# Performance work log

Hardware: AMD Instinct MI355X
Metric: run time of the kernel (lower is better)

The kernel has to match this reference:

```python
import jax, jax.numpy as jnp
import numpy as np

N = 100000   # nodes
E = 1600000  # edges
H = 8        # heads
D = 16       # per-head dim
HD = H * D   # 128 = hidden_dim * num_heads == input_dim
G = 128      # graphs in batch
OUT = 64     # output_dim
EPS = 1e-3   # BatchNorm eps
NEG_SLOPE = 0.2
THRESH = 0.5


def setup_inputs() -> dict:
    key = jax.random.key(0)
    ks = jax.random.split(key, 20)
    rn = lambda k, s: jax.random.normal(k, s, jnp.float32) * 0.1
    return {
        "h": jax.random.normal(ks[0], (N, HD), jnp.float32),
        "src": jax.random.randint(ks[1], (E,), 0, N),
        "dst": jax.random.randint(ks[2], (E,), 0, N),
        "graph_ids": jnp.sort(jax.random.randint(ks[3], (N,), 0, G)),
        # GAT layer 0 params
        "W0": rn(ks[4], (HD, HD)), "al0": rn(ks[5], (H, D)), "ar0": rn(ks[6], (H, D)), "b0": rn(ks[7], (HD,)),
        "g0": jnp.ones((HD,), jnp.float32), "be0": jnp.zeros((HD,), jnp.float32),
        # GAT layer 1 params
        "W1": rn(ks[8], (HD, HD)), "al1": rn(ks[9], (H, D)), "ar1": rn(ks[10], (H, D)), "b1": rn(ks[11], (HD,)),
        "g1": jnp.ones((HD,), jnp.float32), "be1": jnp.zeros((HD,), jnp.float32),
        # MaskLinear prediction head
        "pred_W": rn(ks[12], (OUT, HD)), "pred_b": rn(ks[13], (OUT,)),
        "mask_real": jax.random.uniform(ks[14], (OUT, HD), jnp.float32),
    }


def _gat(h, W, al, ar, b, src, dst):
    # DGL GATConv: fc -> per-node attn halves -> edge LeakyReLU -> segment softmax over dst -> scatter-add
    feat = (h @ W).reshape(N, H, D)                 # [N,H,D]
    el = jnp.sum(feat * al, axis=-1)                # [N,H]
    er = jnp.sum(feat * ar, axis=-1)                # [N,H]
    e = jax.nn.leaky_relu(el[src] + er[dst], NEG_SLOPE)  # [E,H]
    emax = jax.ops.segment_max(e, dst, num_segments=N)   # [N,H]
    ee = jnp.exp(e - emax[dst])
    denom = jax.ops.segment_sum(ee, dst, num_segments=N) # [N,H]
    a = ee / denom[dst]                             # [E,H]
    msg = a[:, :, None] * feat[src]                 # [E,H,D]
    out = jax.ops.segment_sum(msg, dst, num_segments=N)  # [N,H,D]
    return out.reshape(N, HD) + b


def _bn(x, g, be):
    mu = jnp.mean(x, axis=0)
    var = jnp.mean((x - mu) ** 2, axis=0)
    return (x - mu) * jax.lax.rsqrt(var + EPS) * g + be


def reference(h, src, dst, graph_ids, W0, al0, ar0, b0, g0, be0,
              W1, al1, ar1, b1, g1, be1, pred_W, pred_b, mask_real):
    # layer 0: GAT -> BN -> ReLU (no residual)
    h1 = jax.nn.relu(_bn(_gat(h, W0, al0, ar0, b0, src, dst), g0, be0))
    # layer 1: GAT -> BN -> ReLU + residual
    h2 = jax.nn.relu(_bn(_gat(h1, W1, al1, ar1, b1, src, dst), g1, be1)) + h1
    # SumPooling over graphs in the batch
    pooled = jax.ops.segment_sum(h2, graph_ids, num_segments=G)  # [G,HD]
    # MaskLinear with binarized mask (eval path, no dropout)
    mask = (mask_real > THRESH).astype(pooled.dtype)
    return pooled @ (pred_W * mask).T + pred_b  # [G,OUT]
```

## Files before the change

kernel.cpp:

```cpp
#include <hip/hip_runtime.h>
#include <cstdint>

#define N_NODES 100000
#define N_EDGES 1600000
#define H 8
#define D 16
#define HD 128
#define G_GRAPHS 128
#define OUT_DIM 64
#define EPS 1e-3f
#define NEG 0.2f
#define NBUCK 196
#define BSHIFT 9
#define BCAP 10240
#define MT 64
#define APAD 136
#define NTILES 1563
#define GEMM_GRID 512
#define BNP_ROWS 64
#define BNS_ROWS 128
#define WTROWS 144
#define SRCMASK 0x1FFFF

typedef __attribute__((ext_vector_type(8))) short bf16x8;
typedef __attribute__((ext_vector_type(4))) float f32x4;
typedef __attribute__((ext_vector_type(8))) unsigned short u16x8;

__device__ __forceinline__ unsigned short f2bf(float x) {
    unsigned u = __float_as_uint(x);
    unsigned r = (u + 0x7FFFu + ((u >> 16) & 1u)) >> 16;
    return (unsigned short)r;
}
__device__ __forceinline__ float plo(unsigned q) {
    return __uint_as_float(q << 16);
}
__device__ __forceinline__ float phi(unsigned q) {
    return __uint_as_float(q & 0xFFFF0000u);
}
__device__ __forceinline__ unsigned packbf(float a, float b) {
    return (unsigned)f2bf(a) | ((unsigned)f2bf(b) << 16);
}

__global__ void convert_wt(const float* __restrict__ W0, const float* __restrict__ W1,
                           const float* __restrict__ al0, const float* __restrict__ ar0,
                           const float* __restrict__ al1, const float* __restrict__ ar1,
                           unsigned short* __restrict__ Wt0, unsigned short* __restrict__ Wt1,
                           int* __restrict__ bucketCnt, float* __restrict__ pooled,
                           float* __restrict__ sums01) {
    int t = blockIdx.x * blockDim.x + threadIdx.x;
    if (t < NBUCK) bucketCnt[t] = 0;
    if (t < 512) sums01[t] = 0.f;
    for (int i = t; i < G_GRAPHS * HD; i += gridDim.x * blockDim.x) pooled[i] = 0.f;
    if (t < HD * HD) {
        int k = t >> 7, n = t & 127;
        Wt0[n * HD + k] = f2bf(W0[t]);
        Wt1[n * HD + k] = f2bf(W1[t]);
        return;
    }
    int u = t - HD * HD;
    if (u < HD * 16) {
        int k = u >> 4, j = u & 15;
        int h = j & 7;
        const float* a0 = (j < 8) ? al0 : ar0;
        const float* a1 = (j < 8) ? al1 : ar1;
        float s0 = 0.f, s1 = 0.f;
#pragma unroll
        for (int d = 0; d < 16; ++d) {
            s0 += W0[k * HD + h * 16 + d] * a0[h * 16 + d];
            s1 += W1[k * HD + h * 16 + d] * a1[h * 16 + d];
        }
        Wt0[(HD + j) * HD + k] = f2bf(s0);
        Wt1[(HD + j) * HD + k] = f2bf(s1);
    }
}

__global__ __launch_bounds__(256) void bucket_scatter(const int4* __restrict__ src4,
                                                      const int4* __restrict__ dst4,
                                                      int* __restrict__ bucketCnt,
                                                      int* __restrict__ pairs) {
    __shared__ int hist[NBUCK];
    __shared__ int cur[NBUCK];
    int t = threadIdx.x;
    if (t < NBUCK) hist[t] = 0;
    __syncthreads();
    int base4 = blockIdx.x * 1024;
    const int NE4 = N_EDGES / 4;
    int4 s[4], d[4];
    int valid[4];
#pragma unroll
    for (int k = 0; k < 4; ++k) {
        int i4 = base4 + t + k * 256;
        if (i4 < NE4) {
            s[k] = src4[i4];
            d[k] = dst4[i4];
            valid[k] = 1;
            atomicAdd(&hist[d[k].x >> BSHIFT], 1);
            atomicAdd(&hist[d[k].y >> BSHIFT], 1);
            atomicAdd(&hist[d[k].z >> BSHIFT], 1);
            atomicAdd(&hist[d[k].w >> BSHIFT], 1);
        } else {
            valid[k] = 0;
        }
    }
    __syncthreads();
    if (t < NBUCK) {
        int c = hist[t];
        cur[t] = (c > 0) ? atomicAdd(&bucketCnt[t], c) : 0;
    }
    __syncthreads();
#pragma unroll
    for (int k = 0; k < 4; ++k) {
        if (valid[k]) {
            int ss[4] = {s[k].x, s[k].y, s[k].z, s[k].w};
            int dd[4] = {d[k].x, d[k].y, d[k].z, d[k].w};
#pragma unroll
            for (int j = 0; j < 4; ++j) {
                int b = dd[j] >> BSHIFT;
                int slot = atomicAdd(&cur[b], 1);
                pairs[(size_t)b * BCAP + slot] = ((dd[j] & 511) << 17) | ss[j];
            }
        }
    }
}

__global__ __launch_bounds__(256) void bucket_finish(const int* __restrict__ bucketCnt,
                                                     const int* __restrict__ pairs,
                                                     int2* __restrict__ ninfo,
                                                     int* __restrict__ csr_src) {
    __shared__ int hist[512];
    __shared__ int loc[512];
    __shared__ int bufA[256], bufB[256];
    __shared__ int bbase_sh;
    int b = blockIdx.x, t = threadIdx.x;
    int mycnt = bucketCnt[b];
    int base0 = b << BSHIFT;

    bufA[t] = (t < NBUCK) ? bucketCnt[t] : 0;
    __syncthreads();
    {
        int* a = bufA; int* bb = bufB;
        for (int off = 1; off < 256; off <<= 1) {
            int val = a[t];
            if (t >= off) val += a[t - off];
            bb[t] = val;
            __syncthreads();
            int* c = a; a = bb; bb = c;
        }
        if (t == 0) bbase_sh = a[b] - mycnt;
    }
    hist[t] = 0;
    hist[t + 256] = 0;
    __syncthreads();
    {
        const int4* p4 = (const int4*)&pairs[(size_t)b * BCAP];
        int n4 = mycnt >> 2;
        for (int i = t; i < n4; i += 256) {
            int4 w = p4[i];
            atomicAdd(&hist[(unsigned)w.x >> 17], 1);
            atomicAdd(&hist[(unsigned)w.y >> 17], 1);
            atomicAdd(&hist[(unsigned)w.z >> 17], 1);
            atomicAdd(&hist[(unsigned)w.w >> 17], 1);
        }
        for (int i = (n4 << 2) + t; i < mycnt; i += 256)
            atomicAdd(&hist[(unsigned)pairs[(size_t)b * BCAP + i] >> 17], 1);
    }
    __syncthreads();
    int s0 = hist[2 * t], s1 = hist[2 * t + 1];
    int ps = s0 + s1;
    bufA[t] = ps;
    __syncthreads();
    int total_excl;
    {
        int* a = bufA; int* bb = bufB;
        for (int off = 1; off < 256; off <<= 1) {
            int val = a[t];
            if (t >= off) val += a[t - off];
            bb[t] = val;
            __syncthreads();
            int* c = a; a = bb; bb = c;
        }
        total_excl = a[t] - ps;
    }
    int bbase = bbase_sh;
    loc[2 * t] = total_excl;
    loc[2 * t + 1] = total_excl + s0;
    int n0 = base0 + 2 * t, n1 = base0 + 2 * t + 1;
    if (n0 < N_NODES) ninfo[n0] = make_int2(bbase + total_excl, s0);
    if (n1 < N_NODES) ninfo[n1] = make_int2(bbase + total_excl + s0, s1);
    __syncthreads();
    {
        const int4* p4 = (const int4*)&pairs[(size_t)b * BCAP];
        int n4 = mycnt >> 2;
        for (int i = t; i < n4; i += 256) {
            int4 w = p4[i];
            int ws[4] = {w.x, w.y, w.z, w.w};
#pragma unroll
            for (int j = 0; j < 4; ++j) {
                int dl = (unsigned)ws[j] >> 17;
                int r = atomicAdd(&loc[dl], 1);
                csr_src[bbase + r] = ws[j] & SRCMASK;
            }
        }
        for (int i = (n4 << 2) + t; i < mycnt; i += 256) {
            int w = pairs[(size_t)b * BCAP + i];
            int dl = (unsigned)w >> 17;
            int r = atomicAdd(&loc[dl], 1);
            csr_src[bbase + r] = w & SRCMASK;
        }
    }
}

template <int MODE>
__global__ __launch_bounds__(256, 2) void gemm_mfma(const void* __restrict__ Xv,
                                                    const unsigned short* __restrict__ Wt,
                                                    unsigned short* __restrict__ Yb,
                                                    float* __restrict__ el,
                                                    float* __restrict__ er,
                                                    int nrows,
                                                    const float* __restrict__ sums,
                                                    const float* __restrict__ gam,
                                                    const float* __restrict__ bet) {
    __shared__ unsigned short As[MT * APAD];
    __shared__ __align__(16) float scs[HD];
    __shared__ __align__(16) float shs[HD];
    int tid = threadIdx.x;
    int wave = tid >> 6, lane = tid & 63;
    int qd = lane >> 4, l16 = lane & 15;

    if (MODE == 1) {
        if (tid < HD) {
            float invN = 1.0f / (float)N_NODES;
            float mu = sums[tid] * invN;
            float rs = rsqrtf(sums[HD + tid] * invN - mu * mu + EPS);
            float sc = rs * gam[tid];
            scs[tid] = sc;
            shs[tid] = bet[tid] - mu * sc;
        }
        __syncthreads();
    }

    bf16x8 bfr[9][4];
#pragma unroll
    for (int nt = 0; nt < 9; ++nt)
#pragma unroll
        for (int kb = 0; kb < 4; ++kb)
            bfr[nt][kb] = *(const bf16x8*)&Wt[(nt * 16 + l16) * HD + kb * 32 + qd * 8];

    int srow = tid >> 2, scol = (tid & 3) * 32;

    for (int t = blockIdx.x; t < NTILES; t += gridDim.x) {
        int rbase = t * MT;
        {
            int gr = rbase + srow;
            u16x8 o[4];
            if (gr < nrows) {
                if (MODE == 0) {
                    const float* X = (const float*)Xv;
#pragma unroll
                    for (int i = 0; i < 4; ++i) {
                        float4 va = *(const float4*)&X[(size_t)gr * HD + scol + i * 8];
                        float4 vb = *(const float4*)&X[(size_t)gr * HD + scol + i * 8 + 4];
                        o[i][0] = f2bf(va.x); o[i][1] = f2bf(va.y);
                        o[i][2] = f2bf(va.z); o[i][3] = f2bf(va.w);
                        o[i][4] = f2bf(vb.x); o[i][5] = f2bf(vb.y);
                        o[i][6] = f2bf(vb.z); o[i][7] = f2bf(vb.w);
                    }
                } else {
                    const unsigned* X32 = (const unsigned*)Xv;
#pragma unroll
                    for (int i = 0; i < 4; ++i) {
                        uint4 u = *(const uint4*)&X32[(size_t)gr * 64 + (scol >> 1) + i * 4];
                        f32x4 sa = *(const f32x4*)&scs[scol + i * 8];
                        f32x4 sb = *(const f32x4*)&scs[scol + i * 8 + 4];
                        f32x4 ha = *(const f32x4*)&shs[scol + i * 8];
                        f32x4 hb = *(const f32x4*)&shs[scol + i * 8 + 4];
                        float z0 = fmaxf(plo(u.x) * sa.x + ha.x, 0.f);
                        float z1 = fmaxf(phi(u.x) * sa.y + ha.y, 0.f);
                        float z2 = fmaxf(plo(u.y) * sa.z + ha.z, 0.f);
                        float z3 = fmaxf(phi(u.y) * sa.w + ha.w, 0.f);
                        float z4 = fmaxf(plo(u.z) * sb.x + hb.x, 0.f);
                        float z5 = fmaxf(phi(u.z) * sb.y + hb.y, 0.f);
                        float z6 = fmaxf(plo(u.w) * sb.z + hb.z, 0.f);
                        float z7 = fmaxf(phi(u.w) * sb.w + hb.w, 0.f);
                        o[i][0] = f2bf(z0); o[i][1] = f2bf(z1);
                        o[i][2] = f2bf(z2); o[i][3] = f2bf(z3);
                        o[i][4] = f2bf(z4); o[i][5] = f2bf(z5);
                        o[i][6] = f2bf(z6); o[i][7] = f2bf(z7);
                    }
                }
            } else {
#pragma unroll
                for (int i = 0; i < 4; ++i) o[i] = (u16x8)0;
            }
#pragma unroll
            for (int i = 0; i < 4; ++i)
                *(u16x8*)&As[srow * APAD + scol + i * 8] = o[i];
        }
        __syncthreads();
        f32x4 acc[9];
#pragma unroll
        for (int nt = 0; nt < 9; ++nt) acc[nt] = (f32x4){0.f, 0.f, 0.f, 0.f};
        bf16x8 afr[4];
#pragma unroll
        for (int kb = 0; kb < 4; ++kb)
            afr[kb] = *(const bf16x8*)&As[(wave * 16 + l16) * APAD + kb * 32 + qd * 8];
#pragma unroll
        for (int nt = 0; nt < 9; ++nt)
#pragma unroll
            for (int kb = 0; kb < 4; ++kb)
                acc[nt] = __builtin_amdgcn_mfma_f32_16x16x32_bf16(afr[kb], bfr[nt][kb], acc[nt], 0, 0, 0);
        int orow = rbase + wave * 16 + qd * 4;
        if (orow + 3 < nrows) {
#pragma unroll
            for (int nt = 0; nt < 8; ++nt)
#pragma unroll
                for (int r = 0; r < 4; ++r)
                    Yb[(size_t)(orow + r) * HD + nt * 16 + l16] = f2bf(acc[nt][r]);
#pragma unroll
            for (int r = 0; r < 4; ++r) {
                float v = acc[8][r];
                if (l16 < 8) el[(orow + r) * 8 + l16] = v;
                else er[(orow + r) * 8 + (l16 - 8)] = v;
            }
        } else {
#pragma unroll
            for (int nt = 0; nt < 8; ++nt)
                for (int r = 0; r < 4; ++r)
                    if (orow + r < nrows)
                        Yb[(size_t)(orow + r) * HD + nt * 16 + l16] = f2bf(acc[nt][r]);
            for (int r = 0; r < 4; ++r) {
                if (orow + r < nrows) {
                    float v = acc[8][r];
                    if (l16 < 8) el[(orow + r) * 8 + l16] = v;
                    else er[(orow + r) * 8 + (l16 - 8)] = v;
                }
            }
        }
        __syncthreads();
    }
}

__global__ __launch_bounds__(256) void gat_node(const int2* __restrict__ ninfo,
                                                const int* __restrict__ csr_src,
                                                const float* __restrict__ el,
                                                const float* __restrict__ er,
                                                const uint2* __restrict__ featq,
                                                unsigned* __restrict__ gatb) {
    int node = blockIdx.x * 4 + (threadIdx.x >> 6);
    if (node >= N_NODES) return;
    int lane = threadIdx.x & 63;
    int h7 = lane & 7;
    int eidx = lane >> 3;
    int l32 = lane & 31;
    int hacc = l32 >> 2;
    int half = lane >> 5;
    int ibase = half * 8 + hacc;

    int2 pd = ninfo[node];
    int p = pd.x;
    int cnt = pd.y;
    float ern = er[node * 8 + h7];
    float ds = 0.f, a0 = 0.f, a1 = 0.f, a2 = 0.f, a3 = 0.f;

    int nfull = cnt & ~7;
    if (nfull) {
        int s = csr_src[p + eidx];
        float x = el[(unsigned)s * 8u + h7];
        int c = 0;
        for (;;) {
            float v = x + ern;
            v = fmaxf(v, NEG * v);
            float e = __expf(v);
            ds += e;
            int cn = c + 8;
            int snext = 0; float xnext = 0.f;
            if (cn < nfull) {
                snext = csr_src[p + cn + eidx];
                xnext = el[(unsigned)snext * 8u + h7];
            }
#pragma unroll
            for (int k = 0; k < 4; ++k) {
                float ek = __shfl(e, ibase + 16 * k);
                int sk = __shfl(s, ibase + 16 * k);
                uint2 q = featq[(size_t)((unsigned)sk * 32u + (unsigned)l32)];
                a0 += ek * plo(q.x); a1 += ek * phi(q.x);
                a2 += ek * plo(q.y); a3 += ek * phi(q.y);
            }
            if (cn >= nfull) break;
            c = cn; s = snext; x = xnext;
        }
    }
    int rem = cnt & 7;
    if (rem) {
        int s = 0; float e = 0.f;
        if (eidx < rem) {
            s = csr_src[p + nfull + eidx];
            float v = el[(unsigned)s * 8u + h7] + ern;
            v = fmaxf(v, NEG * v);
            e = __expf(v);
        }
        ds += e;
        int nst = (rem + 1) >> 1;
        for (int k = 0; k < nst; ++k) {
            float ek = __shfl(e, ibase + 16 * k);
            int sk = __shfl(s, ibase + 16 * k);
            uint2 q = featq[(size_t)((unsigned)sk * 32u + (unsigned)l32)];
            a0 += ek * plo(q.x); a1 += ek * phi(q.x);
            a2 += ek * plo(q.y); a3 += ek * phi(q.y);
        }
    }
    ds += __shfl_xor(ds, 8);
    ds += __shfl_xor(ds, 16);
    ds += __shfl_xor(ds, 32);
    float dfull = __shfl(ds, hacc);
    float invd = dfull > 0.f ? 1.f / dfull : 0.f;
    a0 += __shfl_xor(a0, 32);
    a1 += __shfl_xor(a1, 32);
    a2 += __shfl_xor(a2, 32);
    a3 += __shfl_xor(a3, 32);
    if (half == 0) {
        uint2 w;
        w.x = packbf(a0 * invd, a1 * invd);
        w.y = packbf(a2 * invd, a3 * invd);
        ((uint2*)gatb)[(size_t)node * 32 + l32] = w;
    }
}

__global__ __launch_bounds__(256) void bn_stats(const unsigned* __restrict__ xb,
                                                float* __restrict__ sums, int nrows) {
    int cp = threadIdx.x & 63;
    int rr = threadIdx.x >> 6;
    int r0 = blockIdx.x * BNS_ROWS;
    int rend = r0 + BNS_ROWS < nrows ? r0 + BNS_ROWS : nrows;
    float s0 = 0.f, q0 = 0.f, s1 = 0.f, q1 = 0.f;
    for (int r = r0 + rr; r < rend; r += 4) {
        unsigned u = xb[(size_t)r * 64 + cp];
        float a = plo(u), b = phi(u);
        s0 += a; q0 += a * a;
        s1 += b; q1 += b * b;
    }
    __shared__ float red[4][256];
    red[0][threadIdx.x] = s0;
    red[1][threadIdx.x] = q0;
    red[2][threadIdx.x] = s1;
    red[3][threadIdx.x] = q1;
    __syncthreads();
    if (rr == 0) {
        int c0 = cp * 2, c1 = c0 + 1;
        float ts0 = red[0][cp] + red[0][cp + 64] + red[0][cp + 128] + red[0][cp + 192];
        float tq0 = red[1][cp] + red[1][cp + 64] + red[1][cp + 128] + red[1][cp + 192];
        float ts1 = red[2][cp] + red[2][cp + 64] + red[2][cp + 128] + red[2][cp + 192];
        float tq1 = red[3][cp] + red[3][cp + 64] + red[3][cp + 128] + red[3][cp + 192];
        atomicAdd(&sums[c0], ts0);
        atomicAdd(&sums[128 + c0], tq0);
        atomicAdd(&sums[c1], ts1);
        atomicAdd(&sums[128 + c1], tq1);
    }
}

__global__ __launch_bounds__(256) void bn_pool(const unsigned* __restrict__ gat1,
                                               const float* __restrict__ sums1,
                                               const float* __restrict__ g1v,
                                               const float* __restrict__ be1v,
                                               const unsigned* __restrict__ gat0,
                                               const float* __restrict__ sums0,
                                               const float* __restrict__ g0v,
                                               const float* __restrict__ be0v,
                                               const int* __restrict__ gid,
                                               float* __restrict__ pooled) {
    int cp = threadIdx.x & 63;
    int rr = threadIdx.x >> 6;
    int c0 = cp * 2, c1 = c0 + 1;
    float invN = 1.0f / (float)N_NODES;
    float mu10 = sums1[c0] * invN, mu11 = sums1[c1] * invN;
    float rs10 = rsqrtf(sums1[128 + c0] * invN - mu10 * mu10 + EPS);
    float rs11 = rsqrtf(sums1[128 + c1] * invN - mu11 * mu11 + EPS);
    float A10 = rs10 * g1v[c0], B10 = be1v[c0] - mu10 * A10;
    float A11 = rs11 * g1v[c1], B11 = be1v[c1] - mu11 * A11;
    float mu00 = sums0[c0] * invN, mu01 = sums0[c1] * invN;
    float rs00 = rsqrtf(sums0[128 + c0] * invN - mu00 * mu00 + EPS);
    float rs01 = rsqrtf(sums0[128 + c1] * invN - mu01 * mu01 + EPS);
    float A00 = rs00 * g0v[c0], B00 = be0v[c0] - mu00 * A00;
    float A01 = rs01 * g0v[c1], B01 = be0v[c1] - mu01 * A01;
    int r0 = blockIdx.x * BNP_ROWS;
    int rend = r0 + BNP_ROWS < N_NODES ? r0 + BNP_ROWS : N_NODES;
    int r = r0 + rr;
    if (r >= rend) return;
    float a0 = 0.f, a1 = 0.f;
    int cur = gid[r];
    for (; r < rend; r += 4) {
        int gg = gid[r];
        if (gg != cur) {
            atomicAdd(&pooled[cur * HD + c0], a0);
            atomicAdd(&pooled[cur * HD + c1], a1);
            a0 = a1 = 0.f;
            cur = gg;
        }
        unsigned u = gat1[(size_t)r * 64 + cp];
        float z0 = plo(u) * A10 + B10;
        float z1 = phi(u) * A11 + B11;
        z0 = z0 > 0.f ? z0 : 0.f;
        z1 = z1 > 0.f ? z1 : 0.f;
        unsigned v = gat0[(size_t)r * 64 + cp];
        float h0 = plo(v) * A00 + B00;
        float h1 = phi(v) * A01 + B01;
        h0 = h0 > 0.f ? h0 : 0.f;
        h1 = h1 > 0.f ? h1 : 0.f;
        a0 += z0 + h0;
        a1 += z1 + h1;
    }
    atomicAdd(&pooled[cur * HD + c0], a0);
    atomicAdd(&pooled[cur * HD + c1], a1);
}

__global__ void pred_kernel(const float* __restrict__ pooled, const float* __restrict__ W,
                            const float* __restrict__ b, const float* __restrict__ mask,
                            float* __restrict__ out) {
    int t = blockIdx.x * blockDim.x + threadIdx.x;
    if (t >= G_GRAPHS * OUT_DIM) return;
    int g = t >> 6, o = t & 63;
    float acc = b[o];
#pragma unroll 4
    for (int c = 0; c < HD; ++c) {
        float m = mask[o * HD + c] > 0.5f ? 1.f : 0.f;
        acc += pooled[g * HD + c] * W[o * HD + c] * m;
    }
    out[t] = acc;
}

extern "C" void kernel_launch(void* const* d_in, const int* in_sizes, int n_in,
                              void* d_out, int out_size, void* d_ws, size_t ws_size,
                              hipStream_t stream) {
    const float* h   = (const float*)d_in[0];
    const int*   src = (const int*)d_in[1];
    const int*   dst = (const int*)d_in[2];
    const int*   gid = (const int*)d_in[3];
    const float* W0  = (const float*)d_in[4];
    const float* al0 = (const float*)d_in[5];
    const float* ar0 = (const float*)d_in[6];
    const float* g0  = (const float*)d_in[8];
    const float* be0 = (const float*)d_in[9];
    const float* W1  = (const float*)d_in[10];
    const float* al1 = (const float*)d_in[11];
    const float* ar1 = (const float*)d_in[12];
    const float* g1  = (const float*)d_in[14];
    const float* be1 = (const float*)d_in[15];
    const float* pW  = (const float*)d_in[16];
    const float* pb  = (const float*)d_in[17];
    const float* msk = (const float*)d_in[18];
    float* out = (float*)d_out;

    unsigned short* gat0  = (unsigned short*)d_ws;
    unsigned short* gat1  = gat0 + (size_t)N_NODES * HD;
    unsigned short* featb = gat1 + (size_t)N_NODES * HD;
    float* el   = (float*)(featb + (size_t)N_NODES * HD);
    float* er   = el + (size_t)N_NODES * H;
    int2*  ninfo = (int2*)(er + (size_t)N_NODES * H);
    int*   csr_src = (int*)(ninfo + N_NODES);
    int*   bucketCnt = csr_src + N_EDGES;
    float* sums0  = (float*)(bucketCnt + 256);
    float* sums1  = sums0 + 256;
    float* pooled = sums1 + 256;
    unsigned short* wt0 = (unsigned short*)(pooled + G_GRAPHS * HD);
    unsigned short* wt1 = wt0 + WTROWS * HD;
    int*   pairs  = (int*)gat1;

    const int TB = 256;
    dim3 blk(TB);
    int bsc_blocks  = (N_EDGES + 4095) / 4096;
    int node_blocks = (N_NODES + 3) / 4;
    int bns_blocks  = (N_NODES + BNS_ROWS - 1) / BNS_ROWS;
    int bnp_blocks  = (N_NODES + BNP_ROWS - 1) / BNP_ROWS;
    int cw_blocks   = (HD * HD + HD * 16 + TB - 1) / TB;

    convert_wt<<<cw_blocks, blk, 0, stream>>>(W0, W1, al0, ar0, al1, ar1, wt0, wt1,
                                              bucketCnt, pooled, sums0);
    bucket_scatter<<<bsc_blocks, blk, 0, stream>>>((const int4*)src, (const int4*)dst,
                                                   bucketCnt, pairs);
    bucket_finish<<<NBUCK, blk, 0, stream>>>(bucketCnt, pairs, ninfo, csr_src);

    gemm_mfma<0><<<GEMM_GRID, blk, 0, stream>>>(h, wt0, featb, el, er, N_NODES,
                                                nullptr, nullptr, nullptr);
    gat_node<<<node_blocks, blk, 0, stream>>>(ninfo, csr_src, el, er,
                                              (const uint2*)featb, (unsigned*)gat0);
    bn_stats<<<bns_blocks, blk, 0, stream>>>((const unsigned*)gat0, sums0, N_NODES);

    gemm_mfma<1><<<GEMM_GRID, blk, 0, stream>>>(gat0, wt1, featb, el, er, N_NODES,
                                                sums0, g0, be0);
    gat_node<<<node_blocks, blk, 0, stream>>>(ninfo, csr_src, el, er,
                                              (const uint2*)featb, (unsigned*)gat1);
    bn_stats<<<bns_blocks, blk, 0, stream>>>((const unsigned*)gat1, sums1, N_NODES);
    bn_pool<<<bnp_blocks, blk, 0, stream>>>((const unsigned*)gat1, sums1, g1, be1,
                                            (const unsigned*)gat0, sums0, g0, be0,
                                            gid, pooled);

    pred_kernel<<<(G_GRAPHS * OUT_DIM + TB - 1) / TB, blk, 0, stream>>>(pooled, pW, pb, msk, out);
}
```

Baseline: 466.1 us.

## Double-buffer GEMM A-tile staging to overlap next-tile loads with MFMA compute

The persistent MFMA GEMM now prefetches the next row tile from global memory into registers while the current tile is computed from shared memory. It writes the prefetched tile into a second LDS buffer afterwards, so only one barrier is needed per iteration. The aim is to hide global load latency behind MFMA work and the output stores. In exchange it doubles LDS use for the A tile and holds the prefetch registers live across the compute, which could reduce occupancy.

Measured after the change: 466.3 us. Within noise of the previous version (+0.0%).

```diff
diff --git a/kernel.cpp b/kernel.cpp
--- a/kernel.cpp
+++ b/kernel.cpp
@@ -211,6 +211,51 @@
 }
 
 template <int MODE>
+__device__ __forceinline__ void stage_load(const void* __restrict__ Xv, int gr, int scol,
+                                           int nrows, const float* scs, const float* shs,
+                                           u16x8 o[4]) {
+    if (gr < nrows) {
+        if (MODE == 0) {
+            const float* X = (const float*)Xv;
+#pragma unroll
+            for (int i = 0; i < 4; ++i) {
+                float4 va = *(const float4*)&X[(size_t)gr * HD + scol + i * 8];
+                float4 vb = *(const float4*)&X[(size_t)gr * HD + scol + i * 8 + 4];
+                o[i][0] = f2bf(va.x); o[i][1] = f2bf(va.y);
+                o[i][2] = f2bf(va.z); o[i][3] = f2bf(va.w);
+                o[i][4] = f2bf(vb.x); o[i][5] = f2bf(vb.y);
+                o[i][6] = f2bf(vb.z); o[i][7] = f2bf(vb.w);
+            }
+        } else {
+            const unsigned* X32 = (const unsigned*)Xv;
+#pragma unroll
+            for (int i = 0; i < 4; ++i) {
+                uint4 u = *(const uint4*)&X32[(size_t)gr * 64 + (scol >> 1) + i * 4];
+                f32x4 sa = *(const f32x4*)&scs[scol + i * 8];
+                f32x4 sb = *(const f32x4*)&scs[scol + i * 8 + 4];
+                f32x4 ha = *(const f32x4*)&shs[scol + i * 8];
+                f32x4 hb = *(const f32x4*)&shs[scol + i * 8 + 4];
+                float z0 = fmaxf(plo(u.x) * sa.x + ha.x, 0.f);
+                float z1 = fmaxf(phi(u.x) * sa.y + ha.y, 0.f);
+                float z2 = fmaxf(plo(u.y) * sa.z + ha.z, 0.f);
+                float z3 = fmaxf(phi(u.y) * sa.w + ha.w, 0.f);
+                float z4 = fmaxf(plo(u.z) * sb.x + hb.x, 0.f);
+                float z5 = fmaxf(phi(u.z) * sb.y + hb.y, 0.f);
+                float z6 = fmaxf(plo(u.w) * sb.z + hb.z, 0.f);
+                float z7 = fmaxf(phi(u.w) * sb.w + hb.w, 0.f);
+                o[i][0] = f2bf(z0); o[i][1] = f2bf(z1);
+                o[i][2] = f2bf(z2); o[i][3] = f2bf(z3);
+                o[i][4] = f2bf(z4); o[i][5] = f2bf(z5);
+                o[i][6] = f2bf(z6); o[i][7] = f2bf(z7);
+            }
+        }
+    } else {
+#pragma unroll
+        for (int i = 0; i < 4; ++i) o[i] = (u16x8)0;
+    }
+}
+
+template <int MODE>
 __global__ __launch_bounds__(256, 2) void gemm_mfma(const void* __restrict__ Xv,
                                                     const unsigned short* __restrict__ Wt,
                                                     unsigned short* __restrict__ Yb,
@@ -220,7 +265,7 @@
                                                     const float* __restrict__ sums,
                                                     const float* __restrict__ gam,
                                                     const float* __restrict__ bet) {
-    __shared__ unsigned short As[MT * APAD];
+    __shared__ unsigned short As[2][MT * APAD];
     __shared__ __align__(16) float scs[HD];
     __shared__ __align__(16) float shs[HD];
     int tid = threadIdx.x;
@@ -248,68 +293,33 @@
 
     int srow = tid >> 2, scol = (tid & 3) * 32;
 
-    for (int t = blockIdx.x; t < NTILES; t += gridDim.x) {
-        int rbase = t * MT;
-        {
-            int gr = rbase + srow;
-            u16x8 o[4];
-            if (gr < nrows) {
-                if (MODE == 0) {
-                    const float* X = (const float*)Xv;
-#pragma unroll
-                    for (int i = 0; i < 4; ++i) {
-                        float4 va = *(const float4*)&X[(size_t)gr * HD + scol + i * 8];
-                        float4 vb = *(const float4*)&X[(size_t)gr * HD + scol + i * 8 + 4];
-                        o[i][0] = f2bf(va.x); o[i][1] = f2bf(va.y);
-                        o[i][2] = f2bf(va.z); o[i][3] = f2bf(va.w);
-                        o[i][4] = f2bf(vb.x); o[i][5] = f2bf(vb.y);
-                        o[i][6] = f2bf(vb.z); o[i][7] = f2bf(vb.w);
-                    }
-                } else {
-                    const unsigned* X32 = (const unsigned*)Xv;
-#pragma unroll
-                    for (int i = 0; i < 4; ++i) {
-                        uint4 u = *(const uint4*)&X32[(size_t)gr * 64 + (scol >> 1) + i * 4];
-                        f32x4 sa = *(const f32x4*)&scs[scol + i * 8];
-                        f32x4 sb = *(const f32x4*)&scs[scol + i * 8 + 4];
-                        f32x4 ha = *(const f32x4*)&shs[scol + i * 8];
-                        f32x4 hb = *(const f32x4*)&shs[scol + i * 8 + 4];
-                        float z0 = fmaxf(plo(u.x) * sa.x + ha.x, 0.f);
-                        float z1 = fmaxf(phi(u.x) * sa.y + ha.y, 0.f);
-                        float z2 = fmaxf(plo(u.y) * sa.z + ha.z, 0.f);
-                        float z3 = fmaxf(phi(u.y) * sa.w + ha.w, 0.f);
-                        float z4 = fmaxf(plo(u.z) * sb.x + hb.x, 0.f);
-                        float z5 = fmaxf(phi(u.z) * sb.y + hb.y, 0.f);
-                        float z6 = fmaxf(plo(u.w) * sb.z + hb.z, 0.f);
-                        float z7 = fmaxf(phi(u.w) * sb.w + hb.w, 0.f);
-                        o[i][0] = f2bf(z0); o[i][1] = f2bf(z1);
-                        o[i][2] = f2bf(z2); o[i][3] = f2bf(z3);
-                        o[i][4] = f2bf(z4); o[i][5] = f2bf(z5);
-                        o[i][6] = f2bf(z6); o[i][7] = f2bf(z7);
-                    }
-                }
-            } else {
-#pragma unroll
-                for (int i = 0; i < 4; ++i) o[i] = (u16x8)0;
-            }
-#pragma unroll
-            for (int i = 0; i < 4; ++i)
-                *(u16x8*)&As[srow * APAD + scol + i * 8] = o[i];
-        }
-        __syncthreads();
+    u16x8 o[4];
+    int t = blockIdx.x;
+    stage_load<MODE>(Xv, t * MT + srow, scol, nrows, scs, shs, o);
+#pragma unroll
+    for (int i = 0; i < 4; ++i)
+        *(u16x8*)&As[0][srow * APAD + scol + i * 8] = o[i];
+    __syncthreads();
+    int cur = 0;
+
+    for (; t < NTILES; t += gridDim.x) {
+        int tn = t + (int)gridDim.x;
+        bool more = tn < NTILES;
+        if (more)
+            stage_load<MODE>(Xv, tn * MT + srow, scol, nrows, scs, shs, o);
         f32x4 acc[9];
 #pragma unroll
         for (int nt = 0; nt < 9; ++nt) acc[nt] = (f32x4){0.f, 0.f, 0.f, 0.f};
         bf16x8 afr[4];
 #pragma unroll
         for (int kb = 0; kb < 4; ++kb)
-            afr[kb] = *(const bf16x8*)&As[(wave * 16 + l16) * APAD + kb * 32 + qd * 8];
+            afr[kb] = *(const bf16x8*)&As[cur][(wave * 16 + l16) * APAD + kb * 32 + qd * 8];
 #pragma unroll
         for (int nt = 0; nt < 9; ++nt)
 #pragma unroll
             for (int kb = 0; kb < 4; ++kb)
                 acc[nt] = __builtin_amdgcn_mfma_f32_16x16x32_bf16(afr[kb], bfr[nt][kb], acc[nt], 0, 0, 0);
-        int orow = rbase + wave * 16 + qd * 4;
+        int orow = t * MT + wave * 16 + qd * 4;
         if (orow + 3 < nrows) {
 #pragma unroll
             for (int nt = 0; nt < 8; ++nt)
@@ -336,7 +346,13 @@
                 }
             }
         }
+        if (more) {
+#pragma unroll
+            for (int i = 0; i < 4; ++i)
+                *(u16x8*)&As[cur ^ 1][srow * APAD + scol + i * 8] = o[i];
+        }
         __syncthreads();
+        cur ^= 1;
     }
 }
 
```
